# Kernel tuning notes

Measured on AMD Instinct MI355X. Metric: run time of the kernel, lower is better.

## Reference

```python
import jax, jax.numpy as jnp
import numpy as np

B, S, D, H, FF = 2, 2048, 1024, 16, 4096
DK = D // H
LOCAL_WINDOW, STRIDE = 128, 128
NEG = -1000000000.0
EPS = 1e-5


def _layernorm(x, g, b):
    mu = jnp.mean(x, axis=-1, keepdims=True)
    var = jnp.mean(jnp.square(x - mu), axis=-1, keepdims=True)
    return (x - mu) * jax.lax.rsqrt(var + EPS) * g + b


def _strided_mask(seq):
    # allowed(i, j): j <= i and (i-j <= local_window or (i-j) % stride == 0)
    i = jnp.arange(seq)[:, None]
    j = jnp.arange(seq)[None, :]
    d = i - j
    return (d >= 0) & ((d <= LOCAL_WINDOW) | (d % STRIDE == 0))  # [S, S] bool


def setup_inputs() -> dict:
    key = jax.random.key(0)
    ks = jax.random.split(key, 18)
    w = lambda k, shape: jax.random.normal(k, shape, jnp.float32) * 0.02
    return {
        "x": jax.random.normal(ks[0], (B, S, D), jnp.float32),
        "mask": jnp.ones((1, 1, S, S), jnp.int32),
        "Wq": w(ks[1], (D, D)), "bq": jnp.zeros((D,), jnp.float32),
        "Wk": w(ks[2], (D, D)), "bk": jnp.zeros((D,), jnp.float32),
        "Wv": w(ks[3], (D, D)), "bv": jnp.zeros((D,), jnp.float32),
        "Wo": w(ks[4], (D, D)), "bo": jnp.zeros((D,), jnp.float32),
        "W1": w(ks[5], (D, FF)), "bf1": jnp.zeros((FF,), jnp.float32),
        "W2": w(ks[6], (FF, D)), "bf2": jnp.zeros((D,), jnp.float32),
        "g1": jnp.ones((D,), jnp.float32), "bl1": jnp.zeros((D,), jnp.float32),
        "g2": jnp.ones((D,), jnp.float32), "bl2": jnp.zeros((D,), jnp.float32),
    }


def reference(x, mask, Wq, bq, Wk, bk, Wv, bv, Wo, bo,
              W1, bf1, W2, bf2, g1, bl1, g2, bl2):
    b, s, d = x.shape
    sm = _strided_mask(s)[None, None]  # [1,1,S,S]

    # pre-LN self-attention
    n = _layernorm(x, g1, bl1)
    split = lambda t: t.reshape(b, s, H, DK).transpose(0, 2, 1, 3)  # [B,H,S,DK]
    q = split(n @ Wq + bq)
    k = split(n @ Wk + bk)
    v = split(n @ Wv + bv)

    scores = jnp.einsum('bhqd,bhkd->bhqk', q, k) / jnp.sqrt(jnp.float32(DK))
    scores = jnp.where(sm, scores, NEG)          # strided/local mask
    scores = jnp.where(mask == 0, NEG, scores)   # user mask
    attn = jax.nn.softmax(scores, axis=-1)
    o = jnp.einsum('bhqk,bhkd->bhqd', attn, v)
    o = o.transpose(0, 2, 1, 3).reshape(b, s, d) @ Wo + bo
    x = x + o

    # pre-LN FFN (GELU exact, matching torch nn.GELU default)
    n2 = _layernorm(x, g2, bl2)
    ff = jax.nn.gelu(n2 @ W1 + bf1, approximate=False) @ W2 + bf2
    return x + ff
```

## Files before the change

### kernel.cpp

```cpp
#include <hip/hip_runtime.h>
#include <math.h>

typedef unsigned int u32;
typedef unsigned short u16;

#define B_  2
#define S_  2048
#define D_  1024
#define H_  16
#define DK_ 64
#define FF_ 4096
#define NEG_ -1000000000.0f

typedef __attribute__((ext_vector_type(8))) short short8;
typedef __attribute__((ext_vector_type(4))) float floatx4;
typedef __attribute__((ext_vector_type(4))) unsigned short ushort4_t;

__device__ inline u16 f2b(float f) {
    union { float f; u32 u; } v; v.f = f;
    u32 r = (v.u + 0x7fffu + ((v.u >> 16) & 1u)) >> 16;
    return (u16)r;
}
__device__ inline float b2f(u16 b) {
    union { u32 u; float f; } v; v.u = ((u32)b) << 16;
    return v.f;
}

__device__ inline void gl_lds16(const u16* g, u16* l) {
    __builtin_amdgcn_global_load_lds((const __attribute__((address_space(1))) u32*)g,
                                     (__attribute__((address_space(3))) u32*)l, 16, 0, 0);
}

__global__ void tconv4(const float* __restrict__ W0, const float* __restrict__ W1_,
                       const float* __restrict__ W2_, const float* __restrict__ W3,
                       u16* __restrict__ dstBase) {
    __shared__ float tile[32][33];
    int z = blockIdx.z;
    const float* Wm = (z == 0) ? W0 : (z == 1) ? W1_ : (z == 2) ? W2_ : W3;
    u16* Wt = dstBase + (size_t)z * 1024 * 1024;
    const int K = 1024, N = 1024;
    int n0 = blockIdx.x * 32, k0 = blockIdx.y * 32;
    int tx = threadIdx.x & 31, ty = threadIdx.x >> 5;
#pragma unroll
    for (int r = 0; r < 32; r += 8)
        tile[ty + r][tx] = Wm[(size_t)(k0 + ty + r) * N + n0 + tx];
    __syncthreads();
#pragma unroll
    for (int r = 0; r < 32; r += 8)
        Wt[(size_t)(n0 + ty + r) * K + k0 + tx] = f2b(tile[tx][ty + r]);
}

__global__ void tconv(const float* __restrict__ Wm, u16* __restrict__ Wt, int K, int N) {
    __shared__ float tile[32][33];
    int n0 = blockIdx.x * 32, k0 = blockIdx.y * 32;
    int tx = threadIdx.x & 31, ty = threadIdx.x >> 5;
#pragma unroll
    for (int r = 0; r < 32; r += 8)
        tile[ty + r][tx] = Wm[(size_t)(k0 + ty + r) * N + n0 + tx];
    __syncthreads();
#pragma unroll
    for (int r = 0; r < 32; r += 8)
        Wt[(size_t)(n0 + ty + r) * K + k0 + tx] = f2b(tile[tx][ty + r]);
}

__global__ void catbias(const float* __restrict__ bq, const float* __restrict__ bk,
                        const float* __restrict__ bv, float* __restrict__ out) {
    int i = blockIdx.x * 256 + threadIdx.x;
    float v = (i < 1024) ? bq[i] : (i < 2048) ? bk[i - 1024] : bv[i - 2048];
    out[i] = v;
}

__global__ __launch_bounds__(256)
void mask_tiles(const int* __restrict__ mask, int* __restrict__ tflag) {
    int jt = blockIdx.x, it = blockIdx.y;
    const int* base = mask + (size_t)it * 128 * S_ + jt * 128;
    int t = threadIdx.x;
    int ok = 1;
    for (int e = t; e < 128 * 32; e += 256) {
        int r = e >> 5, c4 = e & 31;
        int4 vv = *(const int4*)&base[(size_t)r * S_ + c4 * 4];
        ok &= (vv.x != 0) & (vv.y != 0) & (vv.z != 0) & (vv.w != 0);
    }
    ok = (int)__all(ok);
    __shared__ int red[4];
    if ((t & 63) == 0) red[t >> 6] = ok;
    __syncthreads();
    if (t == 0) tflag[it * 16 + jt] = red[0] & red[1] & red[2] & red[3];
}

__global__ void ln_bf16(const float* __restrict__ x, const float* __restrict__ g,
                        const float* __restrict__ b, u16* __restrict__ out) {
    int row = blockIdx.x;
    int t = threadIdx.x;
    const float* xr = x + (size_t)row * D_;
    __shared__ float red[256];

    float v[4];
    float s = 0.f;
#pragma unroll
    for (int i = 0; i < 4; i++) { v[i] = xr[i * 256 + t]; s += v[i]; }
    red[t] = s; __syncthreads();
    for (int off = 128; off > 0; off >>= 1) {
        if (t < off) red[t] += red[t + off];
        __syncthreads();
    }
    float mu = red[0] * (1.0f / D_);
    __syncthreads();

    float vs = 0.f;
#pragma unroll
    for (int i = 0; i < 4; i++) { float d = v[i] - mu; vs += d * d; }
    red[t] = vs; __syncthreads();
    for (int off = 128; off > 0; off >>= 1) {
        if (t < off) red[t] += red[t + off];
        __syncthreads();
    }
    float rstd = rsqrtf(red[0] * (1.0f / D_) + 1e-5f);

    u16* outr = out + (size_t)row * D_;
#pragma unroll
    for (int i = 0; i < 4; i++) {
        int col = i * 256 + t;
        outr[col] = f2b((v[i] - mu) * rstd * g[col] + b[col]);
    }
}

__global__ __launch_bounds__(256)
void merge_ln(const u16* __restrict__ P, const float* __restrict__ x,
              const float* __restrict__ bo, const float* __restrict__ g,
              const float* __restrict__ bl, float* __restrict__ x1,
              u16* __restrict__ n2) {
    const size_t MN = (size_t)B_ * S_ * D_;
    int row = blockIdx.x, t = threadIdx.x;
    size_t base = (size_t)row * D_;
    __shared__ float red[256];

    float v[4];
    float s = 0.f;
#pragma unroll
    for (int i = 0; i < 4; i++) {
        int col = i * 256 + t;
        float val = x[base + col] + bo[col] + b2f(P[base + col]) + b2f(P[MN + base + col]);
        v[i] = val; s += val;
    }
    red[t] = s; __syncthreads();
    for (int off = 128; off > 0; off >>= 1) {
        if (t < off) red[t] += red[t + off];
        __syncthreads();
    }
    float mu = red[0] * (1.0f / D_);
    __syncthreads();

    float vs = 0.f;
#pragma unroll
    for (int i = 0; i < 4; i++) { float d = v[i] - mu; vs += d * d; }
    red[t] = vs; __syncthreads();
    for (int off = 128; off > 0; off >>= 1) {
        if (t < off) red[t] += red[t + off];
        __syncthreads();
    }
    float rstd = rsqrtf(red[0] * (1.0f / D_) + 1e-5f);

#pragma unroll
    for (int i = 0; i < 4; i++) {
        int col = i * 256 + t;
        x1[base + col] = v[i];
        n2[base + col] = f2b((v[i] - mu) * rstd * g[col] + bl[col]);
    }
}

#define BARR asm volatile("s_barrier" ::: "memory")
#define WAITL0 do { asm volatile("s_waitcnt lgkmcnt(0)" ::: "memory"); \
                    __builtin_amdgcn_sched_barrier(0); } while (0)

template <int EPI>
__global__ __launch_bounds__(512, 2)
void gemm8(const u16* __restrict__ A, const u16* __restrict__ Bt,
           const float* __restrict__ bias, void* __restrict__ Cv,
           int M, int N, int K, int ldA, int ldB) {
    __shared__ u16 sh2[65536];
    const int tid = threadIdx.x;
    const int lane = tid & 63, w = tid >> 6;
    const int wm = w >> 2, wn = w & 3;
    const int c = lane & 15, g = lane >> 4;
    const int cbase = c * 128 + g * 16;
    const int xo = (c & 7) << 4;

    int nMt = gridDim.x;
    int nwg = gridDim.x * gridDim.y;
    int id = blockIdx.x + nMt * blockIdx.y;
    int qq = nwg >> 3;
    int sid = (id & 7) * qq + (id >> 3);
    int m0 = (sid % nMt) * 256, n0 = (sid / nMt) * 256;
    size_t koff = (size_t)blockIdx.z * K;

    const int nT = K >> 6, nI = nT >> 1;

    const int sr = tid >> 3;
    const int sk = ((tid & 7) * 8) ^ (((tid >> 3) & 7) << 3);
    const u16* gA0 = A + (size_t)(m0 + sr) * ldA + koff + sk;
    const u16* gB0 = Bt + (size_t)(n0 + sr) * ldB + koff + sk;
    const int dst0 = w * 512;

#define STG_A(t_, h_) do { \
    const u16* s_ = gA0 + (size_t)(h_) * 128 * ldA + (t_) * 64; \
    u16* l_ = &sh2[((((t_) & 1) * 2 + (h_)) * 8192) + dst0]; \
    gl_lds16(s_, l_); \
    gl_lds16(s_ + (size_t)64 * ldA, l_ + 4096); \
} while (0)
#define STG_B(t_, h_) do { \
    const u16* s_ = gB0 + (size_t)(h_) * 128 * ldB + (t_) * 64; \
    u16* l_ = &sh2[32768 + ((((t_) & 1) * 2 + (h_)) * 8192) + dst0]; \
    gl_lds16(s_, l_); \
    gl_lds16(s_ + (size_t)64 * ldB, l_ + 4096); \
} while (0)

    short8 fa[8], fb0[4], fb1[4];
    floatx4 acc[2][2][4][2];
#pragma unroll
    for (int i = 0; i < 2; i++)
#pragma unroll
        for (int j = 0; j < 2; j++)
#pragma unroll
            for (int a = 0; a < 4; a++)
#pragma unroll
                for (int b2 = 0; b2 < 2; b2++)
                    acc[i][j][a][b2] = (floatx4){0.f, 0.f, 0.f, 0.f};

#define DS_A(d_, qr_) do { \
    int rb_ = ((d_) * 2 + wm) * 16384; \
    _Pragma("unroll") for (int a_ = 0; a_ < 4; a_++) \
    _Pragma("unroll") for (int k_ = 0; k_ < 2; k_++) { \
        int lin_ = (qr_) * 8192 + a_ * 2048 + cbase + k_ * 64; \
        fa[a_ * 2 + k_] = *(const short8*)((const char*)sh2 + rb_ + (lin_ ^ xo)); } \
} while (0)
#define DS_B(d_, qc_, fb_) do { \
    int rb_ = 65536 + ((d_) * 2 + (wn >> 1)) * 16384; \
    _Pragma("unroll") for (int b_ = 0; b_ < 2; b_++) \
    _Pragma("unroll") for (int k_ = 0; k_ < 2; k_++) { \
        int lin_ = (wn & 1) * 8192 + (qc_) * 4096 + b_ * 2048 + cbase + k_ * 64; \
        fb_[b_ * 2 + k_] = *(const short8*)((const char*)sh2 + rb_ + (lin_ ^ xo)); } \
} while (0)
#define MFMA16(qr_, qc_, fb_) do { \
    __builtin_amdgcn_s_setprio(1); \
    _Pragma("unroll") for (int a_ = 0; a_ < 4; a_++) \
    _Pragma("unroll") for (int b_ = 0; b_ < 2; b_++) \
    _Pragma("unroll") for (int k_ = 0; k_ < 2; k_++) \
        acc[qr_][qc_][a_][b_] = __builtin_amdgcn_mfma_f32_16x16x32_bf16( \
            fa[a_ * 2 + k_], fb_[b_ * 2 + k_], acc[qr_][qc_][a_][b_], 0, 0, 0); \
    __builtin_amdgcn_s_setprio(0); \
} while (0)

    STG_B(0, 0); STG_B(0, 1); STG_A(0, 0); STG_A(0, 1);
    STG_A(1, 0); STG_A(1, 1);
    asm volatile("s_waitcnt vmcnt(4)" ::: "memory");
    BARR;

    for (int it2 = 0; it2 < nI; it2++) {
        const int t1 = 2 * it2 + 1, tn0 = t1 + 1, tn1 = t1 + 2;
        DS_A(0, 0); DS_B(0, 0, fb0);
        STG_B(t1, 0);
        BARR; WAITL0; MFMA16(0, 0, fb0); BARR;
        DS_B(0, 1, fb1);
        STG_B(t1, 1);
        BARR; WAITL0; MFMA16(0, 1, fb1); BARR;
        DS_A(0, 1);
        if (tn0 < nT) STG_B(tn0, 0);
        BARR; WAITL0; MFMA16(1, 1, fb1); BARR;
        if (tn0 < nT) {
            STG_B(tn0, 1);
            asm volatile("s_waitcnt vmcnt(4)" ::: "memory");
        } else {
            asm volatile("s_waitcnt vmcnt(0)" ::: "memory");
        }
        BARR; WAITL0; MFMA16(1, 0, fb0); BARR;
        DS_A(1, 0); DS_B(1, 0, fb0);
        if (tn0 < nT) STG_A(tn0, 0);
        BARR; WAITL0; MFMA16(0, 0, fb0); BARR;
        DS_B(1, 1, fb1);
        if (tn0 < nT) STG_A(tn0, 1);
        BARR; WAITL0; MFMA16(0, 1, fb1); BARR;
        DS_A(1, 1);
        if (tn1 < nT) STG_A(tn1, 0);
        BARR; WAITL0; MFMA16(1, 1, fb1); BARR;
        if (tn1 < nT) STG_A(tn1, 1);
        if (it2 + 1 < nI) asm volatile("s_waitcnt vmcnt(4)" ::: "memory");
        BARR; WAITL0; MFMA16(1, 0, fb0); BARR;
    }

#pragma unroll
    for (int qr = 0; qr < 2; qr++)
#pragma unroll
        for (int qc = 0; qc < 2; qc++)
#pragma unroll
            for (int a = 0; a < 4; a++)
#pragma unroll
                for (int b2 = 0; b2 < 2; b2++) {
                    int mrow = m0 + wm * 128 + qr * 64 + a * 16 + g * 4;
                    int ncol = n0 + wn * 64 + qc * 32 + b2 * 16 + c;
                    float bv = (EPI == 3) ? 0.f : bias[ncol];
#pragma unroll
                    for (int r = 0; r < 4; r++) {
                        int m = mrow + r;
                        float vvv = acc[qr][qc][a][b2][r] + bv;
                        if (EPI == 0) {
                            int which = ncol >> 10, col = ncol & 1023;
                            if (which == 0) vvv *= 0.125f;
                            int bb = m >> 11, ss = m & 2047, hh = col >> 6, dk = col & 63;
                            ((u16*)Cv)[(size_t)which * ((size_t)B_ * S_ * D_) +
                                       ((((size_t)bb * H_ + hh) * S_) + ss) * DK_ + dk] = f2b(vvv);
                        } else if (EPI == 2) {
                            float u = 0.79788456080286536f * fmaf(0.044715f * vvv, vvv * vvv, vvv);
                            float th = 1.f - 2.f / (1.f + __expf(2.f * u));
                            ((u16*)Cv)[(size_t)m * N + ncol] = f2b(0.5f * vvv * (1.f + th));
                        } else {
                            ((u16*)Cv)[(size_t)blockIdx.z * M * N + (size_t)m * N + ncol] = f2b(vvv);
                        }
                    }
                }
#undef STG_A
#undef STG_B
#undef DS_A
#undef DS_B
#undef MFMA16
}

__global__ __launch_bounds__(256)
void ffn2_merge(const u16* __restrict__ P, const float* __restrict__ x1,
                const float* __restrict__ bf2, float* __restrict__ out) {
    const size_t MN = (size_t)B_ * S_ * D_;
    int e = (blockIdx.x * 256 + threadIdx.x) * 4;
    float4 xv = *(const float4*)&x1[e];
    float4 bv = *(const float4*)&bf2[e & 1023];
    float o0 = xv.x + bv.x, o1 = xv.y + bv.y, o2 = xv.z + bv.z, o3 = xv.w + bv.w;
#pragma unroll
    for (int z = 0; z < 4; z++) {
        ushort4_t pv = *(const ushort4_t*)&P[z * MN + e];
        o0 += b2f(pv[0]); o1 += b2f(pv[1]); o2 += b2f(pv[2]); o3 += b2f(pv[3]);
    }
    *(float4*)&out[e] = (float4){o0, o1, o2, o3};
}

#define MAXB_ 14
__global__ __launch_bounds__(256)
void attn4(const u16* __restrict__ q, const u16* __restrict__ k,
           const u16* __restrict__ v, const int* __restrict__ mask,
           const int* __restrict__ tileOK, u16* __restrict__ ob) {
    __shared__ u16 sh[19456];
    u16* Kw = sh;
    u16* Qs = sh + 13824;
    u16* Vh = sh + 12800;

    const int bh = blockIdx.x;
    const int i0 = (31 - blockIdx.y) * 64;
    const int b  = bh >> 4, h = bh & 15;
    const int t  = threadIdx.x;
    const int lane = t & 63, w = t >> 6;
    const int c = lane & 15, g = lane >> 4;
    const int g4 = g * 4;
    const int qloc16 = w * 16;

    const u16* qg = q + ((size_t)bh * S_ + i0) * DK_;
    const u16* kg = k + (size_t)bh * S_ * DK_;
    const u16* vg = v + (size_t)bh * S_ * DK_;

    const int wlo = (i0 >= 128) ? i0 - 128 : 0;
    const int wn  = i0 + 64 - wlo;
    const int nb  = (i0 >= 256) ? (i0 >> 7) - 1 : 0;
    const int jb0 = i0 & 127;
    const int dd0 = i0 - wlo;

    bool allOK = true;
    {
        const int* rowf = tileOK + (i0 >> 7) * 16;
        int jt0 = wlo >> 7, jt1 = (i0 + 63) >> 7;
        for (int jt = jt0; jt <= jt1; jt++) allOK &= (rowf[jt] != 0);
        for (int m = 0; m < nb; m++) allOK &= (rowf[m] != 0);
    }

    for (int e = t; e < 64 * 8; e += 256) {
        int row = e >> 3, dc = e & 7;
        *(short8*)&Qs[row * 72 + dc * 8] = *(const short8*)(qg + row * 64 + dc * 8);
    }
    for (int e = t; e < wn * 8; e += 256) {
        int row = e >> 3, dc = e & 7;
        *(short8*)&Kw[row * 72 + dc * 8] = *(const short8*)(kg + (size_t)(wlo + row) * 64 + dc * 8);
    }
    __syncthreads();

    float sbr[MAXB_];
    {
        short8 qv0 = *(const short8*)&Qs[(qloc16 + c) * 72 + g * 8];
        short8 qv1 = *(const short8*)&Qs[(qloc16 + c) * 72 + 32 + g * 8];
#pragma unroll
        for (int m = 0; m < MAXB_; m++) {
            sbr[m] = NEG_;
            if (m < nb) {
                int jrow = jb0 + (m << 7) + qloc16 + c;
                short8 kv0 = *(const short8*)(kg + (size_t)jrow * 64 + g * 8);
                short8 kv1 = *(const short8*)(kg + (size_t)jrow * 64 + 32 + g * 8);
                float p = 0.f;
#pragma unroll
                for (int i = 0; i < 8; i++) {
                    p += b2f((u16)qv0[i]) * b2f((u16)kv0[i]);
                    p += b2f((u16)qv1[i]) * b2f((u16)kv1[i]);
                }
                p += __shfl_xor(p, 16);
                p += __shfl_xor(p, 32);
                if (!allOK && mask[(size_t)(i0 + qloc16 + c) * S_ + jrow] == 0) p = NEG_;
                sbr[m] = p;
            }
        }
    }

    floatx4 sc[12];
#pragma unroll
    for (int ct = 0; ct < 12; ct++) sc[ct] = (floatx4){0.f, 0.f, 0.f, 0.f};
    {
        short8 fa0 = *(const short8*)&Qs[(qloc16 + c) * 72 + g * 8];
        short8 fa1 = *(const short8*)&Qs[(qloc16 + c) * 72 + 32 + g * 8];
#pragma unroll
        for (int ct = 0; ct < 12; ct++) {
            short8 fb0 = *(const short8*)&Kw[(ct * 16 + c) * 72 + g * 8];
            short8 fb1 = *(const short8*)&Kw[(ct * 16 + c) * 72 + 32 + g * 8];
            sc[ct] = __builtin_amdgcn_mfma_f32_16x16x32_bf16(fa0, fb0, sc[ct], 0, 0, 0);
            sc[ct] = __builtin_amdgcn_mfma_f32_16x16x32_bf16(fa1, fb1, sc[ct], 0, 0, 0);
        }
    }

#pragma unroll
    for (int ct = 0; ct < 12; ct++) {
        int cidx = ct * 16 + c;
        int j = wlo + cidx;
#pragma unroll
        for (int r = 0; r < 4; r++) {
            int qloc = qloc16 + g4 + r;
            int d = dd0 + qloc - cidx;
            bool ok = (d >= 0) && (d <= 128);
            if (ok && !allOK) ok = (mask[(size_t)(i0 + qloc) * S_ + j] != 0);
            sc[ct][r] = ok ? sc[ct][r] : NEG_;
        }
    }

    float mv[4], inv[4];
#pragma unroll
    for (int r = 0; r < 4; r++) {
        float bs[MAXB_];
#pragma unroll
        for (int m = 0; m < MAXB_; m++)
            bs[m] = (m < nb) ? __shfl(sbr[m], g4 + r, 64) : NEG_;
        float mm = -1e30f;
#pragma unroll
        for (int ct = 0; ct < 12; ct++) mm = fmaxf(mm, sc[ct][r]);
        mm = fmaxf(mm, __shfl_xor(mm, 1));
        mm = fmaxf(mm, __shfl_xor(mm, 2));
        mm = fmaxf(mm, __shfl_xor(mm, 4));
        mm = fmaxf(mm, __shfl_xor(mm, 8));
#pragma unroll
        for (int m = 0; m < MAXB_; m++)
            if (m < nb) mm = fmaxf(mm, bs[m]);
        float sum = 0.f;
#pragma unroll
        for (int ct = 0; ct < 12; ct++) {
            float e = __expf(sc[ct][r] - mm);
            sc[ct][r] = e;
            sum += e;
        }
        sum += __shfl_xor(sum, 1);
        sum += __shfl_xor(sum, 2);
        sum += __shfl_xor(sum, 4);
        sum += __shfl_xor(sum, 8);
#pragma unroll
        for (int m = 0; m < MAXB_; m++)
            if (m < nb) sum += __expf(bs[m] - mm);
        mv[r] = mm;
        inv[r] = 1.f / sum;
    }

    __syncthreads();
    u16* P = Kw;
#pragma unroll
    for (int ct = 0; ct < 12; ct++)
#pragma unroll
        for (int r = 0; r < 4; r++)
            P[(qloc16 + g4 + r) * 200 + ct * 16 + c] = f2b(sc[ct][r]);

    for (int e = t; e < 768; e += 256) {
        int dc = e / 96, jl = e - dc * 96;
        short8 val = {0, 0, 0, 0, 0, 0, 0, 0};
        if (jl < wn) val = *(const short8*)(vg + (size_t)(wlo + jl) * 64 + dc * 8);
#pragma unroll
        for (int i = 0; i < 8; i++) Vh[(dc * 8 + i) * 104 + jl] = (u16)val[i];
    }
    __syncthreads();

    floatx4 o[4];
#pragma unroll
    for (int nt = 0; nt < 4; nt++) o[nt] = (floatx4){0.f, 0.f, 0.f, 0.f};
#pragma unroll
    for (int ks = 0; ks < 3; ks++) {
        short8 pa = *(const short8*)&P[(qloc16 + c) * 200 + ks * 32 + g * 8];
#pragma unroll
        for (int nt = 0; nt < 4; nt++) {
            short8 vb = *(const short8*)&Vh[(nt * 16 + c) * 104 + ks * 32 + g * 8];
            o[nt] = __builtin_amdgcn_mfma_f32_16x16x32_bf16(pa, vb, o[nt], 0, 0, 0);
        }
    }

    if (wn > 96) {
        __syncthreads();
        for (int e = t; e < 768; e += 256) {
            int dc = e / 96, jl = e - dc * 96;
            int j2 = 96 + jl;
            short8 val = {0, 0, 0, 0, 0, 0, 0, 0};
            if (j2 < wn) val = *(const short8*)(vg + (size_t)(wlo + j2) * 64 + dc * 8);
#pragma unroll
            for (int i = 0; i < 8; i++) Vh[(dc * 8 + i) * 104 + jl] = (u16)val[i];
        }
        __syncthreads();
#pragma unroll
        for (int ks = 0; ks < 3; ks++) {
            short8 pa = *(const short8*)&P[(qloc16 + c) * 200 + 96 + ks * 32 + g * 8];
#pragma unroll
            for (int nt = 0; nt < 4; nt++) {
                short8 vb = *(const short8*)&Vh[(nt * 16 + c) * 104 + ks * 32 + g * 8];
                o[nt] = __builtin_amdgcn_mfma_f32_16x16x32_bf16(pa, vb, o[nt], 0, 0, 0);
            }
        }
    }

#pragma unroll
    for (int m = 0; m < MAXB_; m++) {
        if (m < nb) {
            int vbase = jb0 + (m << 7) + qloc16 + g4;
            u16 vv[4][4];
#pragma unroll
            for (int r = 0; r < 4; r++)
#pragma unroll
                for (int nt = 0; nt < 4; nt++)
                    vv[r][nt] = vg[(size_t)(vbase + r) * 64 + nt * 16 + c];
#pragma unroll
            for (int r = 0; r < 4; r++) {
                float bs = __shfl(sbr[m], g4 + r, 64);
                float pb = __expf(bs - mv[r]);
#pragma unroll
                for (int nt = 0; nt < 4; nt++)
                    o[nt][r] += pb * b2f(vv[r][nt]);
            }
        }
    }

#pragma unroll
    for (int nt = 0; nt < 4; nt++) {
#pragma unroll
        for (int r = 0; r < 4; r++) {
            int qi = i0 + qloc16 + g4 + r;
            ob[((size_t)b * S_ + qi) * D_ + h * 64 + nt * 16 + c] = f2b(o[nt][r] * inv[r]);
        }
    }
}

extern "C" void kernel_launch(void* const* d_in, const int* in_sizes, int n_in,
                              void* d_out, int out_size, void* d_ws, size_t ws_size,
                              hipStream_t stream) {
    const float* x    = (const float*)d_in[0];
    const int*   mask = (const int*)  d_in[1];
    const float* Wq   = (const float*)d_in[2];
    const float* bq   = (const float*)d_in[3];
    const float* Wk   = (const float*)d_in[4];
    const float* bk   = (const float*)d_in[5];
    const float* Wv   = (const float*)d_in[6];
    const float* bv   = (const float*)d_in[7];
    const float* Wo   = (const float*)d_in[8];
    const float* bo   = (const float*)d_in[9];
    const float* W1   = (const float*)d_in[10];
    const float* bf1  = (const float*)d_in[11];
    const float* W2   = (const float*)d_in[12];
    const float* bf2  = (const float*)d_in[13];
    const float* g1   = (const float*)d_in[14];
    const float* bl1  = (const float*)d_in[15];
    const float* g2   = (const float*)d_in[16];
    const float* bl2  = (const float*)d_in[17];

    char* wsb = (char*)d_ws;
    const size_t MB = 1024 * 1024;
    u16*   WtQKV  = (u16*)(wsb + 0);
    u16*   WtO    = (u16*)(wsb + 6 * MB);
    u16*   Wt1    = (u16*)(wsb + 8 * MB);
    u16*   Wt2    = (u16*)(wsb + 16 * MB);
    u16*   n1b    = (u16*)(wsb + 24 * MB);
    u16*   qkv    = (u16*)(wsb + 32 * MB);
    u16*   obb    = (u16*)(wsb + 56 * MB);
    float* x1     = (float*)(wsb + 32 * MB);
    u16*   ff1b   = (u16*)(wsb + 48 * MB);
    u16*   Ppart  = (u16*)(wsb + 82 * MB);
    u16*   PpartO = (u16*)(wsb + 82 * MB);
    float* bcat   = (float*)(wsb + 114 * MB);
    int*   tflag  = (int*)(wsb + 115 * MB);
    u16*   n2b    = n1b;

    const int M = B_ * S_;
    const size_t SZ = (size_t)B_ * S_ * D_;

    mask_tiles<<<dim3(16, 16), 256, 0, stream>>>(mask, tflag);
    tconv4<<<dim3(32, 32, 4), 256, 0, stream>>>(Wq, Wk, Wv, Wo, WtQKV);
    tconv<<<dim3(128, 32), 256, 0, stream>>>(W1, Wt1, 1024, 4096);
    tconv<<<dim3(32, 128), 256, 0, stream>>>(W2, Wt2, 4096, 1024);
    catbias<<<12, 256, 0, stream>>>(bq, bk, bv, bcat);

    ln_bf16<<<M, 256, 0, stream>>>(x, g1, bl1, n1b);

    gemm8<0><<<dim3(16, 12, 1), 512, 0, stream>>>(n1b, WtQKV, bcat, qkv,
                                                  M, 3072, 1024, 1024, 1024);

    attn4<<<dim3(32, 32), 256, 0, stream>>>(qkv, qkv + SZ, qkv + 2 * SZ, mask, tflag, obb);

    gemm8<3><<<dim3(16, 4, 2), 512, 0, stream>>>(obb, WtO, nullptr, PpartO,
                                                 M, 1024, 512, 1024, 1024);
    merge_ln<<<M, 256, 0, stream>>>(PpartO, x, bo, g2, bl2, x1, n2b);

    gemm8<2><<<dim3(16, 16, 1), 512, 0, stream>>>(n2b, Wt1, bf1, ff1b,
                                                  M, 4096, 1024, 1024, 1024);

    gemm8<3><<<dim3(16, 4, 4), 512, 0, stream>>>(ff1b, Wt2, nullptr, Ppart,
                                                 M, 1024, 1024, 4096, 4096);
    ffn2_merge<<<(int)(SZ / 1024), 256, 0, stream>>>(Ppart, x1, bf2, (float*)d_out);
}
```

Before: 371.9 us.

## Vectorize layernorm kernels with wave-shuffle reductions and drop GEMM pre-MFMA barriers

Both layernorm kernels now process four contiguous elements per thread with float4 and ushort4 loads and stores. They reduce mean and variance with wave shuffles and an 8-entry shared array instead of a 256-entry shared-memory tree with many __syncthreads. In the GEMM main loop, the extra s_barrier plus explicit lgkmcnt(0) wait and sched_barrier before each MFMA block are removed, leaving the compiler to insert LDS waits. This cuts barrier and scheduling overhead in the pipelined GEMM. It risks losing the LDS read/write ordering across waves that the removed barrier gave, since the loads feeding an MFMA may race with the global-to-LDS stores of other waves.

```diff
diff --git a/kernel.cpp b/kernel.cpp
--- a/kernel.cpp
+++ b/kernel.cpp
@@ -88,41 +88,37 @@
     if (t == 0) tflag[it * 16 + jt] = red[0] & red[1] & red[2] & red[3];
 }
 
-__global__ void ln_bf16(const float* __restrict__ x, const float* __restrict__ g,
-                        const float* __restrict__ b, u16* __restrict__ out) {
-    int row = blockIdx.x;
-    int t = threadIdx.x;
+__global__ __launch_bounds__(256)
+void ln_bf16(const float* __restrict__ x, const float* __restrict__ g,
+             const float* __restrict__ b, u16* __restrict__ out) {
+    int row = blockIdx.x, t = threadIdx.x;
+    int lane = t & 63, w = t >> 6;
     const float* xr = x + (size_t)row * D_;
-    __shared__ float red[256];
-
-    float v[4];
-    float s = 0.f;
-#pragma unroll
-    for (int i = 0; i < 4; i++) { v[i] = xr[i * 256 + t]; s += v[i]; }
-    red[t] = s; __syncthreads();
-    for (int off = 128; off > 0; off >>= 1) {
-        if (t < off) red[t] += red[t + off];
-        __syncthreads();
-    }
-    float mu = red[0] * (1.0f / D_);
-    __syncthreads();
-
-    float vs = 0.f;
-#pragma unroll
-    for (int i = 0; i < 4; i++) { float d = v[i] - mu; vs += d * d; }
-    red[t] = vs; __syncthreads();
-    for (int off = 128; off > 0; off >>= 1) {
-        if (t < off) red[t] += red[t + off];
-        __syncthreads();
-    }
-    float rstd = rsqrtf(red[0] * (1.0f / D_) + 1e-5f);
-
-    u16* outr = out + (size_t)row * D_;
-#pragma unroll
-    for (int i = 0; i < 4; i++) {
-        int col = i * 256 + t;
-        outr[col] = f2b((v[i] - mu) * rstd * g[col] + b[col]);
-    }
+    __shared__ float red[8];
+    int col0 = t * 4;
+    float4 xv = *(const float4*)&xr[col0];
+    float v0 = xv.x, v1 = xv.y, v2 = xv.z, v3 = xv.w;
+    float s = v0 + v1 + v2 + v3;
+    s += __shfl_xor(s, 1); s += __shfl_xor(s, 2); s += __shfl_xor(s, 4);
+    s += __shfl_xor(s, 8); s += __shfl_xor(s, 16); s += __shfl_xor(s, 32);
+    if (lane == 0) red[w] = s;
+    __syncthreads();
+    float mu = (red[0] + red[1] + red[2] + red[3]) * (1.0f / D_);
+    float d0 = v0 - mu, d1 = v1 - mu, d2 = v2 - mu, d3 = v3 - mu;
+    float vs = d0 * d0 + d1 * d1 + d2 * d2 + d3 * d3;
+    vs += __shfl_xor(vs, 1); vs += __shfl_xor(vs, 2); vs += __shfl_xor(vs, 4);
+    vs += __shfl_xor(vs, 8); vs += __shfl_xor(vs, 16); vs += __shfl_xor(vs, 32);
+    if (lane == 0) red[4 + w] = vs;
+    __syncthreads();
+    float rstd = rsqrtf((red[4] + red[5] + red[6] + red[7]) * (1.0f / D_) + 1e-5f);
+    float4 gv = *(const float4*)&g[col0];
+    float4 bv = *(const float4*)&b[col0];
+    ushort4_t o;
+    o[0] = f2b(d0 * rstd * gv.x + bv.x);
+    o[1] = f2b(d1 * rstd * gv.y + bv.y);
+    o[2] = f2b(d2 * rstd * gv.z + bv.z);
+    o[3] = f2b(d3 * rstd * gv.w + bv.w);
+    *(ushort4_t*)&out[(size_t)row * D_ + col0] = o;
 }
 
 __global__ __launch_bounds__(256)
@@ -132,46 +128,43 @@
               u16* __restrict__ n2) {
     const size_t MN = (size_t)B_ * S_ * D_;
     int row = blockIdx.x, t = threadIdx.x;
+    int lane = t & 63, w = t >> 6;
     size_t base = (size_t)row * D_;
-    __shared__ float red[256];
-
-    float v[4];
-    float s = 0.f;
-#pragma unroll
-    for (int i = 0; i < 4; i++) {
-        int col = i * 256 + t;
-        float val = x[base + col] + bo[col] + b2f(P[base + col]) + b2f(P[MN + base + col]);
-        v[i] = val; s += val;
-    }
-    red[t] = s; __syncthreads();
-    for (int off = 128; off > 0; off >>= 1) {
-        if (t < off) red[t] += red[t + off];
-        __syncthreads();
-    }
-    float mu = red[0] * (1.0f / D_);
-    __syncthreads();
-
-    float vs = 0.f;
-#pragma unroll
-    for (int i = 0; i < 4; i++) { float d = v[i] - mu; vs += d * d; }
-    red[t] = vs; __syncthreads();
-    for (int off = 128; off > 0; off >>= 1) {
-        if (t < off) red[t] += red[t + off];
-        __syncthreads();
-    }
-    float rstd = rsqrtf(red[0] * (1.0f / D_) + 1e-5f);
-
-#pragma unroll
-    for (int i = 0; i < 4; i++) {
-        int col = i * 256 + t;
-        x1[base + col] = v[i];
-        n2[base + col] = f2b((v[i] - mu) * rstd * g[col] + bl[col]);
-    }
+    __shared__ float red[8];
+    int col0 = t * 4;
+    float4 xv = *(const float4*)&x[base + col0];
+    float4 bv = *(const float4*)&bo[col0];
+    ushort4_t p0 = *(const ushort4_t*)&P[base + col0];
+    ushort4_t p1 = *(const ushort4_t*)&P[MN + base + col0];
+    float v0 = xv.x + bv.x + b2f(p0[0]) + b2f(p1[0]);
+    float v1 = xv.y + bv.y + b2f(p0[1]) + b2f(p1[1]);
+    float v2 = xv.z + bv.z + b2f(p0[2]) + b2f(p1[2]);
+    float v3 = xv.w + bv.w + b2f(p0[3]) + b2f(p1[3]);
+    float s = v0 + v1 + v2 + v3;
+    s += __shfl_xor(s, 1); s += __shfl_xor(s, 2); s += __shfl_xor(s, 4);
+    s += __shfl_xor(s, 8); s += __shfl_xor(s, 16); s += __shfl_xor(s, 32);
+    if (lane == 0) red[w] = s;
+    __syncthreads();
+    float mu = (red[0] + red[1] + red[2] + red[3]) * (1.0f / D_);
+    float d0 = v0 - mu, d1 = v1 - mu, d2 = v2 - mu, d3 = v3 - mu;
+    float vs = d0 * d0 + d1 * d1 + d2 * d2 + d3 * d3;
+    vs += __shfl_xor(vs, 1); vs += __shfl_xor(vs, 2); vs += __shfl_xor(vs, 4);
+    vs += __shfl_xor(vs, 8); vs += __shfl_xor(vs, 16); vs += __shfl_xor(vs, 32);
+    if (lane == 0) red[4 + w] = vs;
+    __syncthreads();
+    float rstd = rsqrtf((red[4] + red[5] + red[6] + red[7]) * (1.0f / D_) + 1e-5f);
+    float4 gv = *(const float4*)&g[col0];
+    float4 blv = *(const float4*)&bl[col0];
+    *(float4*)&x1[base + col0] = (float4){v0, v1, v2, v3};
+    ushort4_t o;
+    o[0] = f2b(d0 * rstd * gv.x + blv.x);
+    o[1] = f2b(d1 * rstd * gv.y + blv.y);
+    o[2] = f2b(d2 * rstd * gv.z + blv.z);
+    o[3] = f2b(d3 * rstd * gv.w + blv.w);
+    *(ushort4_t*)&n2[base + col0] = o;
 }
 
 #define BARR asm volatile("s_barrier" ::: "memory")
-#define WAITL0 do { asm volatile("s_waitcnt lgkmcnt(0)" ::: "memory"); \
-                    __builtin_amdgcn_sched_barrier(0); } while (0)
 
 template <int EPI>
 __global__ __launch_bounds__(512, 2)
@@ -260,32 +253,32 @@
         const int t1 = 2 * it2 + 1, tn0 = t1 + 1, tn1 = t1 + 2;
         DS_A(0, 0); DS_B(0, 0, fb0);
         STG_B(t1, 0);
-        BARR; WAITL0; MFMA16(0, 0, fb0); BARR;
+        MFMA16(0, 0, fb0); BARR;
         DS_B(0, 1, fb1);
         STG_B(t1, 1);
-        BARR; WAITL0; MFMA16(0, 1, fb1); BARR;
+        MFMA16(0, 1, fb1); BARR;
         DS_A(0, 1);
         if (tn0 < nT) STG_B(tn0, 0);
-        BARR; WAITL0; MFMA16(1, 1, fb1); BARR;
+        MFMA16(1, 1, fb1); BARR;
         if (tn0 < nT) {
             STG_B(tn0, 1);
             asm volatile("s_waitcnt vmcnt(4)" ::: "memory");
         } else {
             asm volatile("s_waitcnt vmcnt(0)" ::: "memory");
         }
-        BARR; WAITL0; MFMA16(1, 0, fb0); BARR;
+        MFMA16(1, 0, fb0); BARR;
         DS_A(1, 0); DS_B(1, 0, fb0);
         if (tn0 < nT) STG_A(tn0, 0);
-        BARR; WAITL0; MFMA16(0, 0, fb0); BARR;
+        MFMA16(0, 0, fb0); BARR;
         DS_B(1, 1, fb1);
         if (tn0 < nT) STG_A(tn0, 1);
-        BARR; WAITL0; MFMA16(0, 1, fb1); BARR;
+        MFMA16(0, 1, fb1); BARR;
         DS_A(1, 1);
         if (tn1 < nT) STG_A(tn1, 0);
-        BARR; WAITL0; MFMA16(1, 1, fb1); BARR;
+        MFMA16(1, 1, fb1); BARR;
         if (tn1 < nT) STG_A(tn1, 1);
         if (it2 + 1 < nI) asm volatile("s_waitcnt vmcnt(4)" ::: "memory");
-        BARR; WAITL0; MFMA16(1, 0, fb0); BARR;
+        MFMA16(1, 0, fb0); BARR;
     }
 
 #pragma unroll
```

Measured after the change: 365.1 us. No clear change (-1.8%).
